# Optimization experiments

Hardware: AMD Instinct MI355X
Metric: run time of the kernel (lower is better)

## Reference

```python
import jax, jax.numpy as jnp
import numpy as np

B, N, C, K = 8, 2048, 64, 32
RADIUS = 0.2
DENSITY_K = 16
INTRINSIC_DIM = 3
NORMALIZE_DP = True
EPS = 1e-8
BN_EPS = 1e-5


def _cdist(x, y):
    # safe euclidean cdist: (..., I, C), (..., J, C) -> (..., I, J)
    d2 = (jnp.sum(x * x, -1)[..., :, None] + jnp.sum(y * y, -1)[..., None, :]
          - 2.0 * jnp.einsum('...ic,...jc->...ij', x, y))
    d2 = jnp.maximum(d2, 0.0)
    safe = jnp.where(d2 > 0, d2, 1.0)
    return jnp.where(d2 > 0, jnp.sqrt(safe), 0.0)


def _ball_query(coords):
    dists = _cdist(coords, coords)                      # (B,N,N)
    _, knn_idx = jax.lax.top_k(-dists, K)               # k smallest
    masked = jnp.where(dists > RADIUS, jnp.inf, dists)
    neg_vals, m_idx = jax.lax.top_k(-masked, K)
    valid = jnp.isfinite(-neg_vals)
    return jnp.where(valid, m_idx, knn_idx)             # (B,N,K)


def _density_weights(grouped):
    # grouped: (B,M,K,3)
    gd = _cdist(grouped, grouped)                       # (B,M,K,K)
    eye = jnp.eye(K, dtype=bool)
    gd = jnp.where(eye, jnp.inf, gd)
    kth = -jax.lax.top_k(-gd, DENSITY_K)[0][..., -1]    # (B,M,K) k-th NN dist
    raw = jnp.maximum(kth, EPS) ** INTRINSIC_DIM
    return raw / jnp.maximum(jnp.sum(raw, -1, keepdims=True), EPS)


def setup_inputs() -> dict:
    key = jax.random.key(0)
    k1, k2, k3 = jax.random.split(key, 3)
    return {
        'coords': jax.random.uniform(k1, (B, N, 3), dtype=jnp.float32),
        'feats': jax.random.normal(k2, (B, C, N), dtype=jnp.float32),
        'conv_w': jax.random.normal(k3, (C, C + 3), dtype=jnp.float32) * 0.05,
        'bn_gamma': jnp.ones((C,), jnp.float32),
        'bn_beta': jnp.zeros((C,), jnp.float32),
        'bn_mean': jnp.zeros((C,), jnp.float32),
        'bn_var': jnp.ones((C,), jnp.float32),
    }


def reference(coords, feats, conv_w, bn_gamma, bn_beta, bn_mean, bn_var):
    idx = _ball_query(coords)                                   # (B,N,K)
    grouped_coords = jax.vmap(lambda c, i: c[i])(coords, idx)   # (B,N,K,3)
    rel = grouped_coords - coords[:, :, None, :]
    if NORMALIZE_DP and RADIUS > 0:
        rel = rel / RADIUS
    grouped_feats = jax.vmap(lambda f, i: f[:, i])(feats, idx)  # (B,C,N,K)
    x = jnp.concatenate([jnp.transpose(rel, (0, 3, 1, 2)), grouped_feats], axis=1)  # (B,C+3,N,K)
    y = jnp.einsum('oc,bcmk->bomk', conv_w, x)                  # 1x1 conv, no bias
    inv = bn_gamma / jnp.sqrt(bn_var + BN_EPS)
    y = y * inv[None, :, None, None] + (bn_beta - bn_mean * inv)[None, :, None, None]
    y = jax.nn.relu(y)
    w = _density_weights(grouped_coords)                        # (B,N,K)
    return jnp.sum(y * w[:, None, :, :], axis=-1)               # (B,C,N)
```

## Files before the change

### kernel.cpp

```cpp
#include <hip/hip_runtime.h>
#include <stdint.h>

#define BB 8
#define NN 2048
#define CC 64
#define KK 32
#define DK 16
#define RADIUSF 0.2f
#define EPSF 1e-8f
#define BN_EPSF 1e-5f

typedef unsigned long long u64;
typedef unsigned int u32;

__device__ __forceinline__ float refsq3(float a, float b, float c) {
  return __fadd_rn(__fadd_rn(__fmul_rn(a, a), __fmul_rn(b, b)), __fmul_rn(c, c));
}
__device__ __forceinline__ float refdot3(float ax, float ay, float az,
                                         float bx, float by, float bz) {
  return __builtin_fmaf(az, bz, __builtin_fmaf(ay, by, __fmul_rn(ax, bx)));
}
__device__ __forceinline__ float refdist(float sx, float sy, float dt) {
  float d2 = __fsub_rn(__fadd_rn(sx, sy), __fmul_rn(2.0f, dt));
  d2 = fmaxf(d2, 0.0f);
  return d2 > 0.0f ? __fsqrt_rn(d2) : 0.0f;
}

#define WAVE_SORT64(V)                                                        \
  {                                                                           \
    _Pragma("unroll") for (int k_ = 2; k_ <= 64; k_ <<= 1) {                  \
      _Pragma("unroll") for (int j_ = k_ >> 1; j_ >= 1; j_ >>= 1) {           \
        __typeof__(V) o_ = __shfl_xor(V, j_);                                 \
        bool keepmin_ = ((lane & k_) == 0) == ((lane & j_) == 0);             \
        __typeof__(V) mn_ = V < o_ ? V : o_;                                  \
        __typeof__(V) mx_ = V < o_ ? o_ : V;                                  \
        V = keepmin_ ? mn_ : mx_;                                             \
      }                                                                       \
    }                                                                         \
  }

__global__ __launch_bounds__(256) void pack_kernel(const float* __restrict__ coords,
                                                   float4* __restrict__ P) {
  int t = blockIdx.x * 256 + threadIdx.x;
  float x = coords[t * 3 + 0], y = coords[t * 3 + 1], z = coords[t * 3 + 2];
  P[t] = make_float4(x, y, z, refsq3(x, y, z));
}

__global__ __launch_bounds__(256) void gfeat_kernel(
    const float* __restrict__ feats, const float* __restrict__ conv_w,
    const float* __restrict__ gamma, const float* __restrict__ beta,
    const float* __restrict__ mean, const float* __restrict__ var,
    float* __restrict__ G) {
  __shared__ float wlds[64 * 65];
  for (int e = threadIdx.x; e < 4096; e += 256) {
    int c = e >> 6, cp = e & 63;
    wlds[c * 65 + cp] = conv_w[c * (CC + 3) + 3 + cp];
  }
  __syncthreads();
  int t = blockIdx.x * 256 + threadIdx.x;
  int c = t & 63;
  int m = t >> 6;
  int b = m >> 11;
  int n = m & (NN - 1);
  float inv = __fdiv_rn(gamma[c], __fsqrt_rn(__fadd_rn(var[c], BN_EPSF)));
  float shift = __fsub_rn(beta[c], __fmul_rn(mean[c], inv));
  const float* f = feats + (size_t)b * CC * NN + n;
  float acc = 0.f;
#pragma unroll
  for (int cp = 0; cp < CC; ++cp) acc = fmaf(wlds[c * 65 + cp], f[(size_t)cp * NN], acc);
  G[t] = fmaf(inv, acc, shift);
}

__global__ __launch_bounds__(256) void knn_kernel(const float4* __restrict__ P,
                                                  int* __restrict__ idx_out) {
  __shared__ u64 surv[4 * 64];
  const int lane = threadIdx.x & 63;
  const int wv = threadIdx.x >> 6;
  const int pid = blockIdx.x * 4 + wv;
  const int b = pid >> 11;
  const int i = pid & (NN - 1);
  const float4* Pb = P + ((size_t)b << 11);
  float4 q = Pb[i];
  u64* sv = surv + wv * 64;
  const u64 lml = (1ull << lane) - 1ull;

  u32 du[32];
  u32 m0 = 0xFFFFFFFFu;
#pragma unroll
  for (int c = 0; c < 32; ++c) {
    int j = (c << 6) | lane;
    float4 p = Pb[j];
    float dt = refdot3(q.x, q.y, q.z, p.x, p.y, p.z);
    u32 d = __float_as_uint(refdist(q.w, p.w, dt));
    du[c] = d;
    m0 = d < m0 ? d : m0;
  }

  u32 Av = m0;
  WAVE_SORT64(Av);
  const u32 T = __shfl(Av, 31);

  u32 cls = 0;
#pragma unroll
  for (int c = 0; c < 32; ++c) cls += (du[c] <= T) ? 1u : 0u;
  u32 v2 = cls;
#pragma unroll
  for (int sft = 1; sft < 64; sft <<= 1) {
    u32 o = __shfl_up(v2, sft, 64);
    if (lane >= sft) v2 += o;
  }
  const u32 ntot = __shfl(v2, 63);
  int* op = idx_out + (size_t)pid * KK;

  if (ntot <= 64) {
    u32 pos = v2 - cls;
#pragma unroll
    for (int c = 0; c < 32; ++c) {
      if (du[c] <= T) {
        sv[pos] = ((u64)du[c] << 32) | (u64)(u32)((c << 6) | lane);
        ++pos;
      }
    }
    u64 x = (lane < (int)ntot) ? sv[lane] : ~0ull;
    WAVE_SORT64(x);
    if (lane < KK) op[lane] = (int)((u32)x & 0x7FFu);
  } else {
    u32 ans = 0;
#pragma unroll 1
    for (int bbit = 30; bbit >= 0; --bbit) {
      u32 t2 = ans | (1u << bbit);
      u32 c2 = 0;
#pragma unroll
      for (int c = 0; c < 32; ++c) c2 += (du[c] < t2) ? 1u : 0u;
#pragma unroll
      for (int sft = 1; sft < 64; sft <<= 1) c2 += __shfl_xor(c2, sft);
      if (c2 < KK) ans = t2;
    }
    const u32 D = ans;
    u32 cntL = 0;
#pragma unroll
    for (int c = 0; c < 32; ++c) cntL += (du[c] < D) ? 1u : 0u;
    u32 vL = cntL;
#pragma unroll
    for (int sft = 1; sft < 64; sft <<= 1) {
      u32 o = __shfl_up(vL, sft, 64);
      if (lane >= sft) vL += o;
    }
    const u32 r = KK - __shfl(vL, 63);
    u32 pos = vL - cntL;
#pragma unroll
    for (int c = 0; c < 32; ++c) {
      if (du[c] < D) { op[pos] = (c << 6) | lane; ++pos; }
    }
    u32 emit = r;
    u32 wpos = KK - r;
#pragma unroll
    for (int c = 0; c < 32; ++c) {
      if (emit != 0) {
        u64 mk = __ballot(du[c] == D);
        u32 pc = (u32)__popcll(mk);
        u32 rk = (u32)__popcll(mk & lml);
        if ((du[c] == D) && rk < emit) op[wpos + rk] = (c << 6) | lane;
        u32 take = pc < emit ? pc : emit;
        wpos += take;
        emit -= take;
      }
    }
  }
}

__global__ __launch_bounds__(256) void dagg_kernel(
    const float4* __restrict__ P, const float* __restrict__ conv_w,
    const float* __restrict__ gamma, const float* __restrict__ var,
    const float* __restrict__ G, const int* __restrict__ idxb,
    float* __restrict__ out) {
  __shared__ float4 ldsRW[4][64];
  __shared__ int ldsJ[4][64];
  const int lane = threadIdx.x & 63;
  const int wv = threadIdx.x >> 6;
  const int half = lane >> 5;
  const int k = lane & 31;
  const int pid_pair = blockIdx.x * 8 + wv * 2;
  const int pid = pid_pair + half;
  const int b = pid >> 11;
  const float4* Pb = P + ((size_t)b << 11);

  const int i = pid & (NN - 1);
  float4 q = Pb[i];
  int jk = idxb[(size_t)pid * KK + k];
  float4 nb = Pb[jk];

  float rx = __fdiv_rn(__fsub_rn(nb.x, q.x), RADIUSF);
  float ry = __fdiv_rn(__fsub_rn(nb.y, q.y), RADIUSF);
  float rz = __fdiv_rn(__fsub_rn(nb.z, q.z), RADIUSF);

  u32 d2b[32];
#pragma unroll
  for (int t = 0; t < 32; ++t) {
    float ox = __shfl(nb.x, t, 32);
    float oy = __shfl(nb.y, t, 32);
    float oz = __shfl(nb.z, t, 32);
    float so = __shfl(nb.w, t, 32);
    float dt = refdot3(nb.x, nb.y, nb.z, ox, oy, oz);
    float d2 = __fsub_rn(__fadd_rn(nb.w, so), __fmul_rn(2.0f, dt));
    d2 = fmaxf(d2, 0.0f);
    d2b[t] = (t == k) ? 0x7F800000u : __float_as_uint(d2);
  }
#pragma unroll
  for (int p = 1; p < 32; p <<= 1) {
#pragma unroll
    for (int kk = p; kk >= 1; kk >>= 1) {
#pragma unroll
      for (int jj = (kk & (p - 1)); jj + kk < 32; jj += 2 * kk) {
#pragma unroll
        for (int t = 0; t < kk; ++t) {
          if ((t + jj) / (2 * p) == (t + jj + kk) / (2 * p)) {
            u32 a = d2b[t + jj], b2 = d2b[t + jj + kk];
            d2b[t + jj] = a < b2 ? a : b2;
            d2b[t + jj + kk] = a < b2 ? b2 : a;
          }
        }
      }
    }
  }
  float kd2 = __uint_as_float(d2b[DK - 1]);
  float kth = kd2 > 0.f ? __fsqrt_rn(kd2) : 0.f;
  float r1 = fmaxf(kth, EPSF);
  float raw = __fmul_rn(__fmul_rn(r1, r1), r1);
  float s = raw;
#pragma unroll
  for (int t = 1; t < 32; t <<= 1) s += __shfl_xor(s, t, 32);
  float wk = raw / fmaxf(s, EPSF);

  ldsRW[wv][lane] = make_float4(rx, ry, rz, wk);
  ldsJ[wv][lane] = jk * 64;

  float inv = __fdiv_rn(gamma[lane], __fsqrt_rn(__fadd_rn(var[lane], BN_EPSF)));
  float w0 = conv_w[lane * (CC + 3) + 0] * inv;
  float w1 = conv_w[lane * (CC + 3) + 1] * inv;
  float w2 = conv_w[lane * (CC + 3) + 2] * inv;
  const float* Gb = G + ((size_t)b * NN) * 64 + lane;

#pragma unroll
  for (int h2 = 0; h2 < 2; ++h2) {
    const int pid2 = pid_pair + h2;
    const int i2 = pid2 & (NN - 1);
    float acc = 0.f;
#pragma unroll
    for (int kk2 = 0; kk2 < KK; ++kk2) {
      float4 rw = ldsRW[wv][h2 * 32 + kk2];
      int joff = ldsJ[wv][h2 * 32 + kk2];
      float g = Gb[joff];
      float y = fmaf(w2, rw.z, fmaf(w1, rw.y, fmaf(w0, rw.x, g)));
      y = fmaxf(y, 0.f);
      acc = fmaf(rw.w, y, acc);
    }
    out[((size_t)(b * 64 + lane)) * NN + i2] = acc;
  }
}

extern "C" void kernel_launch(void* const* d_in, const int* in_sizes, int n_in,
                              void* d_out, int out_size, void* d_ws, size_t ws_size,
                              hipStream_t stream) {
  const float* coords = (const float*)d_in[0];
  const float* feats  = (const float*)d_in[1];
  const float* conv_w = (const float*)d_in[2];
  const float* gamma  = (const float*)d_in[3];
  const float* beta   = (const float*)d_in[4];
  const float* mean   = (const float*)d_in[5];
  const float* var    = (const float*)d_in[6];
  float* out = (float*)d_out;

  int*   idxb = (int*)d_ws;
  float4* P   = (float4*)((char*)d_ws + (size_t)2 * 1024 * 1024);
  float* G    = (float*)((char*)d_ws + (size_t)4 * 1024 * 1024);

  const int NPTS = BB * NN;

  pack_kernel<<<NPTS / 256, 256, 0, stream>>>(coords, P);
  knn_kernel<<<NPTS / 4, 256, 0, stream>>>(P, idxb);
  gfeat_kernel<<<(NPTS * CC) / 256, 256, 0, stream>>>(feats, conv_w, gamma, beta,
                                                      mean, var, G);
  dagg_kernel<<<NPTS / 8, 256, 0, stream>>>(P, conv_w, gamma, var, G, idxb, out);
}
```

Measured before the change: 81.65 us.

## Stage batch points in LDS and process multiple queries per kNN block

The kNN kernel now copies all 2048 packed points of a batch into shared memory once per block and loops over 16 queries per block (4 per wave), instead of re-reading them from global memory for every query. It no longer keeps the 32-entry per-lane distance array in registers: it recomputes distances from LDS, takes the threshold from squared distances, and compacts candidates with an LDS atomic counter instead of a prefix scan. This is meant to cut global/L2 traffic and register pressure. In exchange it adds repeated distance computation and a 32KB LDS footprint per block, which can limit occupancy.

New measurement: 96.10 us. 17.7% more time.

```diff
diff --git a/kernel.cpp b/kernel.cpp
--- a/kernel.cpp
+++ b/kernel.cpp
@@ -9,6 +9,7 @@
 #define RADIUSF 0.2f
 #define EPSF 1e-8f
 #define BN_EPSF 1e-5f
+#define QPB 16
 
 typedef unsigned long long u64;
 typedef unsigned int u32;
@@ -24,6 +25,10 @@
   float d2 = __fsub_rn(__fadd_rn(sx, sy), __fmul_rn(2.0f, dt));
   d2 = fmaxf(d2, 0.0f);
   return d2 > 0.0f ? __fsqrt_rn(d2) : 0.0f;
+}
+__device__ __forceinline__ u32 dist_bits(float4 q, float4 p) {
+  float dt = refdot3(q.x, q.y, q.z, p.x, p.y, p.z);
+  return __float_as_uint(refdist(q.w, p.w, dt));
 }
 
 #define WAVE_SORT64(V)                                                        \
@@ -73,97 +78,105 @@
 
 __global__ __launch_bounds__(256) void knn_kernel(const float4* __restrict__ P,
                                                   int* __restrict__ idx_out) {
-  __shared__ u64 surv[4 * 64];
+  __shared__ float4 Pl[NN];
+  __shared__ u64 strip[4][64];
+  __shared__ u32 cnt[4];
   const int lane = threadIdx.x & 63;
   const int wv = threadIdx.x >> 6;
-  const int pid = blockIdx.x * 4 + wv;
-  const int b = pid >> 11;
-  const int i = pid & (NN - 1);
+  const int qbase = blockIdx.x * QPB;
+  const int b = qbase >> 11;
   const float4* Pb = P + ((size_t)b << 11);
-  float4 q = Pb[i];
-  u64* sv = surv + wv * 64;
-  const u64 lml = (1ull << lane) - 1ull;
-
-  u32 du[32];
-  u32 m0 = 0xFFFFFFFFu;
-#pragma unroll
-  for (int c = 0; c < 32; ++c) {
-    int j = (c << 6) | lane;
-    float4 p = Pb[j];
-    float dt = refdot3(q.x, q.y, q.z, p.x, p.y, p.z);
-    u32 d = __float_as_uint(refdist(q.w, p.w, dt));
-    du[c] = d;
-    m0 = d < m0 ? d : m0;
-  }
-
-  u32 Av = m0;
-  WAVE_SORT64(Av);
-  const u32 T = __shfl(Av, 31);
-
-  u32 cls = 0;
-#pragma unroll
-  for (int c = 0; c < 32; ++c) cls += (du[c] <= T) ? 1u : 0u;
-  u32 v2 = cls;
-#pragma unroll
-  for (int sft = 1; sft < 64; sft <<= 1) {
-    u32 o = __shfl_up(v2, sft, 64);
-    if (lane >= sft) v2 += o;
-  }
-  const u32 ntot = __shfl(v2, 63);
-  int* op = idx_out + (size_t)pid * KK;
-
-  if (ntot <= 64) {
-    u32 pos = v2 - cls;
+
+  for (int t = threadIdx.x; t < NN; t += 256) Pl[t] = Pb[t];
+  __syncthreads();
+
+#pragma unroll 1
+  for (int qi = 0; qi < QPB / 4; ++qi) {
+    const int pid = qbase + wv * 4 + qi;
+    const int i = pid & (NN - 1);
+    float4 q = Pl[i];
+
+    u32 m2 = 0xFFFFFFFFu;
 #pragma unroll
     for (int c = 0; c < 32; ++c) {
-      if (du[c] <= T) {
-        sv[pos] = ((u64)du[c] << 32) | (u64)(u32)((c << 6) | lane);
-        ++pos;
-      }
-    }
-    u64 x = (lane < (int)ntot) ? sv[lane] : ~0ull;
-    WAVE_SORT64(x);
-    if (lane < KK) op[lane] = (int)((u32)x & 0x7FFu);
-  } else {
-    u32 ans = 0;
+      float4 p = Pl[(c << 6) | lane];
+      float dt = refdot3(q.x, q.y, q.z, p.x, p.y, p.z);
+      float d2 = __fsub_rn(__fadd_rn(q.w, p.w), __fmul_rn(2.0f, dt));
+      d2 = fmaxf(d2, 0.0f);
+      u32 s = __float_as_uint(d2);
+      m2 = s < m2 ? s : m2;
+    }
+    u32 Av = m2;
+    WAVE_SORT64(Av);
+    u32 t2 = __shfl(Av, 31);
+    float t2f = __uint_as_float(t2);
+    const u32 T = (t2f > 0.f) ? __float_as_uint(__fsqrt_rn(t2f)) : 0u;
+
+    if (lane == 0) cnt[wv] = 0;
+
+#pragma unroll
+    for (int c = 0; c < 32; ++c) {
+      int j = (c << 6) | lane;
+      u32 d = dist_bits(q, Pl[j]);
+      if (d <= T) {
+        u32 slot = atomicAdd(&cnt[wv], 1u);
+        if (slot < 64) strip[wv][slot] = ((u64)d << 32) | (u32)j;
+      }
+    }
+    u32 ntot = cnt[wv];
+    int* op = idx_out + (size_t)pid * KK;
+
+    if (ntot <= 64) {
+      u64 x = (lane < (int)ntot) ? strip[wv][lane] : ~0ull;
+      WAVE_SORT64(x);
+      if (lane < KK) op[lane] = (int)((u32)x & 0x7FFu);
+    } else {
+      u32 ans = 0;
 #pragma unroll 1
-    for (int bbit = 30; bbit >= 0; --bbit) {
-      u32 t2 = ans | (1u << bbit);
-      u32 c2 = 0;
-#pragma unroll
-      for (int c = 0; c < 32; ++c) c2 += (du[c] < t2) ? 1u : 0u;
-#pragma unroll
-      for (int sft = 1; sft < 64; sft <<= 1) c2 += __shfl_xor(c2, sft);
-      if (c2 < KK) ans = t2;
-    }
-    const u32 D = ans;
-    u32 cntL = 0;
-#pragma unroll
-    for (int c = 0; c < 32; ++c) cntL += (du[c] < D) ? 1u : 0u;
-    u32 vL = cntL;
-#pragma unroll
-    for (int sft = 1; sft < 64; sft <<= 1) {
-      u32 o = __shfl_up(vL, sft, 64);
-      if (lane >= sft) vL += o;
-    }
-    const u32 r = KK - __shfl(vL, 63);
-    u32 pos = vL - cntL;
-#pragma unroll
-    for (int c = 0; c < 32; ++c) {
-      if (du[c] < D) { op[pos] = (c << 6) | lane; ++pos; }
-    }
-    u32 emit = r;
-    u32 wpos = KK - r;
-#pragma unroll
-    for (int c = 0; c < 32; ++c) {
-      if (emit != 0) {
-        u64 mk = __ballot(du[c] == D);
-        u32 pc = (u32)__popcll(mk);
-        u32 rk = (u32)__popcll(mk & lml);
-        if ((du[c] == D) && rk < emit) op[wpos + rk] = (c << 6) | lane;
-        u32 take = pc < emit ? pc : emit;
-        wpos += take;
-        emit -= take;
+      for (int bbit = 30; bbit >= 0; --bbit) {
+        u32 t3 = ans | (1u << bbit);
+        u32 c2 = 0;
+#pragma unroll
+        for (int c = 0; c < 32; ++c)
+          c2 += (dist_bits(q, Pl[(c << 6) | lane]) < t3) ? 1u : 0u;
+#pragma unroll
+        for (int sft = 1; sft < 64; sft <<= 1) c2 += __shfl_xor(c2, sft);
+        if (c2 < KK) ans = t3;
+      }
+      const u32 D = ans;
+      u32 cntL = 0;
+#pragma unroll
+      for (int c = 0; c < 32; ++c)
+        cntL += (dist_bits(q, Pl[(c << 6) | lane]) < D) ? 1u : 0u;
+      u32 vL = cntL;
+#pragma unroll
+      for (int sft = 1; sft < 64; sft <<= 1) {
+        u32 o = __shfl_up(vL, sft, 64);
+        if (lane >= sft) vL += o;
+      }
+      const u32 r = KK - __shfl(vL, 63);
+      u32 pos = vL - cntL;
+#pragma unroll
+      for (int c = 0; c < 32; ++c) {
+        int j = (c << 6) | lane;
+        if (dist_bits(q, Pl[j]) < D) { op[pos] = j; ++pos; }
+      }
+      const u64 lml = (1ull << lane) - 1ull;
+      u32 emit = r;
+      u32 wpos = KK - r;
+#pragma unroll
+      for (int c = 0; c < 32; ++c) {
+        if (emit != 0) {
+          int j = (c << 6) | lane;
+          bool eq = dist_bits(q, Pl[j]) == D;
+          u64 mk = __ballot(eq);
+          u32 pc = (u32)__popcll(mk);
+          u32 rk = (u32)__popcll(mk & lml);
+          if (eq && rk < emit) op[wpos + rk] = j;
+          u32 take = pc < emit ? pc : emit;
+          wpos += take;
+          emit -= take;
+        }
       }
     }
   }
@@ -278,7 +291,7 @@
   const int NPTS = BB * NN;
 
   pack_kernel<<<NPTS / 256, 256, 0, stream>>>(coords, P);
-  knn_kernel<<<NPTS / 4, 256, 0, stream>>>(P, idxb);
+  knn_kernel<<<NPTS / QPB, 256, 0, stream>>>(P, idxb);
   gfeat_kernel<<<(NPTS * CC) / 256, 256, 0, stream>>>(feats, conv_w, gamma, beta,
                                                       mean, var, G);
   dagg_kernel<<<NPTS / 8, 256, 0, stream>>>(P, conv_w, gamma, var, G, idxb, out);
```
